# Performance work log

Hardware: AMD Instinct MI355X
Metric: run time of the kernel (lower is better)

Reference implementation:

```python
import jax, jax.numpy as jnp
import numpy as np

N, E = 10000, 320000
MUL0, MUL1 = 64, 32  # 64x0e + 32x1o
SQ3 = 3.0 ** 0.5
SQ2 = 2.0 ** 0.5


def ssp(v):  # shifted softplus
    return jax.nn.softplus(v) - jnp.log(2.0)


def mlp2(v, W1, W2):  # e3nn FullyConnectedNet style: /sqrt(fan_in), no bias, act between
    h = ssp(v @ (W1 / jnp.sqrt(1.0 * W1.shape[0])))
    return h @ (W2 / jnp.sqrt(1.0 * W2.shape[0]))


def linear_rs(x0, x1, W0, b0, W1):  # per-irrep-type linear with 1/sqrt(fan_in) rescale
    y0 = x0 @ (W0 / jnp.sqrt(1.0 * W0.shape[0])) + b0
    y1 = jnp.einsum('nui,uv->nvi', x1, W1) / jnp.sqrt(1.0 * W1.shape[0])
    return y0, y1


def forward(x, edge_sh, edge_attr, W0p, b0p, W1p, W0n, b0n, W1n, G1, g1b, G2, g2b, F1, F2, L1, L2, WO0, bO0, WO1, WO2, edge_index):
    dst, src = edge_index[0], edge_index[1]
    x0 = x[:, :MUL0]                      # [N,64] scalars
    x1 = x[:, MUL0:].reshape(N, MUL1, 3)  # [N,32,3] l=1 vectors
    # linear_node_pre, then invariant edge features s0 (scalars of dst/src + l1 inner products)
    p0, p1 = linear_rs(x0, x1, W0p, b0p, W1p)
    ip1 = jnp.sum(p1[dst] * p1[src], -1) / SQ3          # [E,32]
    s0 = jnp.concatenate([p0[dst], p0[src], ip1], -1)   # [E,160]
    # NormGate: gate scalars + l1 norms through a 2-layer SiLU MLP
    n1 = jnp.sqrt(jnp.sum(x1 * x1, -1) + 1e-12)         # [N,32]
    f0 = jnp.concatenate([x0, n1], -1)                  # [N,96]
    g = jax.nn.silu(f0 @ G1 + g1b) @ G2 + g2b           # [N,96]
    x0g, x1g = g[:, :MUL0], x1 * g[:, MUL0:, None]
    # linear_node
    x0n, x1n = linear_rs(x0g, x1g, W0n, b0n, W1n)
    # per-edge tensor-product weights: fc_node(edge_attr) * layer_l0(s0)
    w = mlp2(edge_attr, F1, F2) * mlp2(s0, L1, L2)      # [E,224]
    w1, w2, w3, w4, w5 = w[:, :64], w[:, 64:128], w[:, 128:160], w[:, 160:192], w[:, 192:224]
    xs0, xs1 = x0n[src], x1n[src]                       # gather source nodes
    sh0, sh1 = edge_sh[:, 0], edge_sh[:, 1:4]
    # depthwise 'uvu' tensor product paths (w3j constants for l<=1)
    o0a = w1 * xs0 * sh0[:, None]                                        # (0e,0e)->0e  [E,64]
    o0b = w4 * jnp.sum(xs1 * sh1[:, None, :], -1) / SQ3                  # (1o,1o)->0e  [E,32]
    o1a = w2[:, :, None] * xs0[:, :, None] * sh1[:, None, :] / SQ3       # (0e,1o)->1o  [E,64,3]
    o1b = w3[:, :, None] * xs1 * sh0[:, None, None]                      # (1o,0e)->1o  [E,32,3]
    o1c = w5[:, :, None] * jnp.cross(xs1, jnp.broadcast_to(sh1[:, None, :], xs1.shape)) / SQ2  # (1o,1o)->1e [E,32,3]
    ef = jnp.concatenate([o0a, o0b, o1a.reshape(E, -1), o1b.reshape(E, -1), o1c.reshape(E, -1)], -1)  # [E,480]
    out = jax.ops.segment_sum(ef, dst, num_segments=N)  # scatter-add over dst
    # linear_out: 96x0e + 96x1o + 32x1e -> 128x0e + 64x1o + 32x1e
    t0 = out[:, :96]
    t1 = out[:, 96:384].reshape(N, 96, 3)
    t2 = out[:, 384:].reshape(N, 32, 3)
    y0 = t0 @ (WO0 / jnp.sqrt(96.0)) + bO0
    y1 = jnp.einsum('nui,uv->nvi', t1, WO1) / jnp.sqrt(96.0)
    y2 = jnp.einsum('nui,uv->nvi', t2, WO2) / jnp.sqrt(32.0)
    return jnp.concatenate([y0, y1.reshape(N, -1), y2.reshape(N, -1)], -1)  # [N,416]


def setup_inputs():
    key = jax.random.key(0)
    ks = jax.random.split(key, 20)
    rn = lambda k, s: jax.random.normal(k, s, dtype=jnp.float32)
    z = lambda n: jnp.zeros((n,), jnp.float32)
    return dict(
        x=rn(ks[0], (N, 160)),
        edge_sh=rn(ks[1], (E, 4)),
        edge_attr=rn(ks[2], (E, 32)),
        W0p=rn(ks[3], (64, 64)), b0p=z(64), W1p=rn(ks[4], (32, 32)),
        W0n=rn(ks[5], (64, 64)), b0n=z(64), W1n=rn(ks[6], (32, 32)),
        G1=rn(ks[7], (96, 96)) / 96 ** 0.5, g1b=z(96),
        G2=rn(ks[8], (96, 96)) / 96 ** 0.5, g2b=z(96),
        F1=rn(ks[9], (32, 32)), F2=rn(ks[10], (32, 224)),
        L1=rn(ks[11], (160, 32)), L2=rn(ks[12], (32, 224)),
        WO0=rn(ks[13], (96, 128)), bO0=z(128),
        WO1=rn(ks[14], (96, 64)), WO2=rn(ks[15], (32, 32)),
        edge_index=jax.random.randint(ks[16], (2, E), 0, N),
    )


def reference(x, edge_sh, edge_attr, W0p, b0p, W1p, W0n, b0n, W1n, G1, g1b, G2, g2b, F1, F2, L1, L2, WO0, bO0, WO1, WO2, edge_index):
    return forward(x, edge_sh, edge_attr, W0p, b0p, W1p, W0n, b0n, W1n, G1, g1b, G2, g2b, F1, F2, L1, L2, WO0, bO0, WO1, WO2, edge_index)
```

## Files before the change

kernel.cpp:

```cpp
#include <hip/hip_runtime.h>
#include <math.h>

#define NN 10000
#define EE 320000
#define TILE 32

constexpr float INVS32  = 0.17677669529663687f;
constexpr float INVS160 = 0.07905694150420949f;
constexpr float INVS96  = 0.10206207261596575f;
constexpr float INVS3   = 0.5773502691896258f;
constexpr float INVS2   = 0.7071067811865476f;
constexpr float LN2     = 0.6931471805599453f;

typedef short bf16x8 __attribute__((ext_vector_type(8)));
typedef float f32x4  __attribute__((ext_vector_type(4)));

__device__ __forceinline__ float sspf(float v) {
  return fmaxf(v, 0.f) + __logf(1.f + __expf(-fabsf(v))) - LN2;
}
__device__ __forceinline__ ushort f2bf(float f) {
  union { float f; unsigned u; } v; v.f = f;
  unsigned r = v.u + 0x7FFF + ((v.u >> 16) & 1);
  return (ushort)(r >> 16);
}
__device__ __forceinline__ float bf2f(ushort u) {
  return __uint_as_float(((unsigned)u) << 16);
}
__device__ __forceinline__ unsigned pk(float a, float b) {
  return (unsigned)f2bf(a) | ((unsigned)f2bf(b) << 16);
}

__global__ __launch_bounds__(1024) void scan_k(const int* __restrict__ cnt,
                                               int* __restrict__ cursor) {
  __shared__ int s[1024];
  const int t = threadIdx.x;
  int loc[10];
  int sum = 0;
#pragma unroll
  for (int jj = 0; jj < 10; ++jj) {
    int idx = t * 10 + jj;
    int c = (idx < NN) ? cnt[idx] : 0;
    loc[jj] = sum;
    sum += c;
  }
  s[t] = sum;
  __syncthreads();
  for (int d = 1; d < 1024; d <<= 1) {
    int v = (t >= d) ? s[t - d] : 0;
    __syncthreads();
    s[t] += v;
    __syncthreads();
  }
  const int excl = (t > 0) ? s[t - 1] : 0;
#pragma unroll
  for (int jj = 0; jj < 10; ++jj) {
    int idx = t * 10 + jj;
    if (idx < NN) cursor[idx] = excl + loc[jj];
  }
}

__global__ void prep_t_k(const float* __restrict__ F2, const float* __restrict__ L2,
                         const float* __restrict__ WO0, const float* __restrict__ WO1,
                         const float* __restrict__ WO2,
                         const float* __restrict__ F1, const float* __restrict__ L1,
                         const int* __restrict__ ei, int* __restrict__ cnt,
                         ushort* __restrict__ F2Tb, ushort* __restrict__ L2Tb,
                         float* __restrict__ WO0T, float* __restrict__ WO1T,
                         float* __restrict__ WO2T,
                         ushort* __restrict__ F1Tb, ushort* __restrict__ L1cTb) {
  int i = blockIdx.x * 256 + threadIdx.x;
  if (i < EE) atomicAdd(&cnt[ei[i]], 1);
  if (i < 7168) {
    int c = i >> 5, k = i & 31;
    float sc = (c < 64)  ? (1.f / 32.f)
             : (c < 128) ? (INVS3 / 32.f)
             : (c < 160) ? (1.f / 32.f)
             : (c < 192) ? (INVS3 / 32.f)
                         : (INVS2 / 32.f);
    F2Tb[i] = f2bf(F2[k * 224 + c] * sc);
    L2Tb[i] = f2bf(L2[k * 224 + c]);
  } else if (i < 7168 + 12288) {
    int j = i - 7168; int k = j / 96, u = j - k * 96;
    WO0T[j] = WO0[u * 128 + k] * INVS96;
  } else if (i < 7168 + 12288 + 6144) {
    int j = i - 7168 - 12288; int v = j / 96, u = j - v * 96;
    WO1T[j] = WO1[u * 64 + v] * INVS96;
  } else if (i < 7168 + 12288 + 6144 + 1024) {
    int j = i - 7168 - 12288 - 6144; int v = j >> 5, u = j & 31;
    WO2T[j] = WO2[u * 32 + v] * INVS32;
  } else if (i < 26624 + 1024) {
    int j = i - 26624; int n = j >> 5, k = j & 31;
    F1Tb[j] = f2bf(F1[k * 32 + n] * INVS32);
  } else if (i < 27648 + 1024) {
    int j = i - 27648; int n = j >> 5, k = j & 31;
    L1cTb[j] = f2bf(L1[(128 + k) * 32 + n] * INVS160);
  }
}

__global__ __launch_bounds__(64) void node_prep_k(
    const float* __restrict__ x,
    const float* __restrict__ W0p, const float* __restrict__ b0p,
    const float* __restrict__ W1p,
    const float* __restrict__ W0n, const float* __restrict__ b0n,
    const float* __restrict__ W1n,
    const float* __restrict__ G1, const float* __restrict__ g1b,
    const float* __restrict__ G2, const float* __restrict__ g2b,
    const float* __restrict__ L1,
    const int* __restrict__ ei, int* __restrict__ cursor, int* __restrict__ order,
    float* __restrict__ p1w, ushort* __restrict__ x0nb, ushort* __restrict__ x1nb,
    float* __restrict__ Aw, float* __restrict__ Bw)
{
  {
    int gid = blockIdx.x * 64 + threadIdx.x;
#pragma unroll
    for (int r = 0; r < 2; ++r) {
      int e = gid + r * 160000;
      int p = atomicAdd(&cursor[ei[e]], 1);
      order[p] = e;
    }
  }

  const int lane = threadIdx.x;
  const int nb = blockIdx.x * 4;

  __shared__ float sX[4][160];
  __shared__ float sP0[4][64];
  __shared__ float sF0[4][96];
  __shared__ float sH1[4][96];
  __shared__ float sG[4][96];

#pragma unroll
  for (int j = 0; j < 4; ++j) {
    const int n = nb + j;
    sX[j][lane]      = x[n * 160 + lane];
    sX[j][lane + 64] = x[n * 160 + lane + 64];
    if (lane < 32) sX[j][lane + 128] = x[n * 160 + lane + 128];
  }

  {
    float a0 = 0.f, a1 = 0.f, a2 = 0.f, a3 = 0.f;
    for (int i = 0; i < 64; ++i) {
      const float w = W0p[i * 64 + lane];
      a0 = fmaf(sX[0][i], w, a0); a1 = fmaf(sX[1][i], w, a1);
      a2 = fmaf(sX[2][i], w, a2); a3 = fmaf(sX[3][i], w, a3);
    }
    const float b = b0p[lane];
    sP0[0][lane] = a0 * 0.125f + b; sP0[1][lane] = a1 * 0.125f + b;
    sP0[2][lane] = a2 * 0.125f + b; sP0[3][lane] = a3 * 0.125f + b;
#pragma unroll
    for (int j = 0; j < 4; ++j) sF0[j][lane] = sX[j][lane];
  }

  {
    const int o = lane; const int v = o / 3, i_ = o - 3 * v;
    float a0 = 0.f, a1 = 0.f, a2 = 0.f, a3 = 0.f;
    for (int u = 0; u < 32; ++u) {
      const float w = W1p[u * 32 + v];
      a0 = fmaf(sX[0][64 + u * 3 + i_], w, a0);
      a1 = fmaf(sX[1][64 + u * 3 + i_], w, a1);
      a2 = fmaf(sX[2][64 + u * 3 + i_], w, a2);
      a3 = fmaf(sX[3][64 + u * 3 + i_], w, a3);
    }
    p1w[(size_t)(nb + 0) * 96 + o] = a0 * INVS32;
    p1w[(size_t)(nb + 1) * 96 + o] = a1 * INVS32;
    p1w[(size_t)(nb + 2) * 96 + o] = a2 * INVS32;
    p1w[(size_t)(nb + 3) * 96 + o] = a3 * INVS32;
  }
  if (lane < 32) {
    const int o = 64 + lane; const int v = o / 3, i_ = o - 3 * v;
    float a0 = 0.f, a1 = 0.f, a2 = 0.f, a3 = 0.f;
    for (int u = 0; u < 32; ++u) {
      const float w = W1p[u * 32 + v];
      a0 = fmaf(sX[0][64 + u * 3 + i_], w, a0);
      a1 = fmaf(sX[1][64 + u * 3 + i_], w, a1);
      a2 = fmaf(sX[2][64 + u * 3 + i_], w, a2);
      a3 = fmaf(sX[3][64 + u * 3 + i_], w, a3);
    }
    p1w[(size_t)(nb + 0) * 96 + o] = a0 * INVS32;
    p1w[(size_t)(nb + 1) * 96 + o] = a1 * INVS32;
    p1w[(size_t)(nb + 2) * 96 + o] = a2 * INVS32;
    p1w[(size_t)(nb + 3) * 96 + o] = a3 * INVS32;
  }

  if (lane < 32) {
#pragma unroll
    for (int j = 0; j < 4; ++j) {
      float s2 = 1e-12f;
#pragma unroll
      for (int i = 0; i < 3; ++i) { float t = sX[j][64 + lane * 3 + i]; s2 += t * t; }
      sF0[j][64 + lane] = sqrtf(s2);
    }
  }

  {
    const float b = g1b[lane];
    float a0 = b, a1 = b, a2 = b, a3 = b;
    for (int i = 0; i < 96; ++i) {
      const float w = G1[i * 96 + lane];
      a0 = fmaf(sF0[0][i], w, a0); a1 = fmaf(sF0[1][i], w, a1);
      a2 = fmaf(sF0[2][i], w, a2); a3 = fmaf(sF0[3][i], w, a3);
    }
    sH1[0][lane] = a0 / (1.f + __expf(-a0));
    sH1[1][lane] = a1 / (1.f + __expf(-a1));
    sH1[2][lane] = a2 / (1.f + __expf(-a2));
    sH1[3][lane] = a3 / (1.f + __expf(-a3));
  }
  if (lane < 32) {
    const int o = 64 + lane;
    const float b = g1b[o];
    float a0 = b, a1 = b, a2 = b, a3 = b;
    for (int i = 0; i < 96; ++i) {
      const float w = G1[i * 96 + o];
      a0 = fmaf(sF0[0][i], w, a0); a1 = fmaf(sF0[1][i], w, a1);
      a2 = fmaf(sF0[2][i], w, a2); a3 = fmaf(sF0[3][i], w, a3);
    }
    sH1[0][o] = a0 / (1.f + __expf(-a0));
    sH1[1][o] = a1 / (1.f + __expf(-a1));
    sH1[2][o] = a2 / (1.f + __expf(-a2));
    sH1[3][o] = a3 / (1.f + __expf(-a3));
  }

  {
    const float b = g2b[lane];
    float a0 = b, a1 = b, a2 = b, a3 = b;
    for (int i = 0; i < 96; ++i) {
      const float w = G2[i * 96 + lane];
      a0 = fmaf(sH1[0][i], w, a0); a1 = fmaf(sH1[1][i], w, a1);
      a2 = fmaf(sH1[2][i], w, a2); a3 = fmaf(sH1[3][i], w, a3);
    }
    sG[0][lane] = a0; sG[1][lane] = a1; sG[2][lane] = a2; sG[3][lane] = a3;
  }
  if (lane < 32) {
    const int o = 64 + lane;
    const float b = g2b[o];
    float a0 = b, a1 = b, a2 = b, a3 = b;
    for (int i = 0; i < 96; ++i) {
      const float w = G2[i * 96 + o];
      a0 = fmaf(sH1[0][i], w, a0); a1 = fmaf(sH1[1][i], w, a1);
      a2 = fmaf(sH1[2][i], w, a2); a3 = fmaf(sH1[3][i], w, a3);
    }
    sG[0][o] = a0; sG[1][o] = a1; sG[2][o] = a2; sG[3][o] = a3;
  }

  {
    float a0 = 0.f, a1 = 0.f, a2 = 0.f, a3 = 0.f;
    for (int i = 0; i < 64; ++i) {
      const float w = W0n[i * 64 + lane];
      a0 = fmaf(sG[0][i], w, a0); a1 = fmaf(sG[1][i], w, a1);
      a2 = fmaf(sG[2][i], w, a2); a3 = fmaf(sG[3][i], w, a3);
    }
    const float b = b0n[lane];
    x0nb[(size_t)(nb + 0) * 64 + lane] = f2bf(a0 * 0.125f + b);
    x0nb[(size_t)(nb + 1) * 64 + lane] = f2bf(a1 * 0.125f + b);
    x0nb[(size_t)(nb + 2) * 64 + lane] = f2bf(a2 * 0.125f + b);
    x0nb[(size_t)(nb + 3) * 64 + lane] = f2bf(a3 * 0.125f + b);
  }

  {
    const int o = lane; const int v = o / 3, i_ = o - 3 * v;
    float a0 = 0.f, a1 = 0.f, a2 = 0.f, a3 = 0.f;
    for (int u = 0; u < 32; ++u) {
      const float w = W1n[u * 32 + v];
      a0 = fmaf(sX[0][64 + u * 3 + i_] * sG[0][64 + u], w, a0);
      a1 = fmaf(sX[1][64 + u * 3 + i_] * sG[1][64 + u], w, a1);
      a2 = fmaf(sX[2][64 + u * 3 + i_] * sG[2][64 + u], w, a2);
      a3 = fmaf(sX[3][64 + u * 3 + i_] * sG[3][64 + u], w, a3);
    }
    x1nb[(size_t)(nb + 0) * 96 + o] = f2bf(a0 * INVS32);
    x1nb[(size_t)(nb + 1) * 96 + o] = f2bf(a1 * INVS32);
    x1nb[(size_t)(nb + 2) * 96 + o] = f2bf(a2 * INVS32);
    x1nb[(size_t)(nb + 3) * 96 + o] = f2bf(a3 * INVS32);
  }
  if (lane < 32) {
    const int o = 64 + lane; const int v = o / 3, i_ = o - 3 * v;
    float a0 = 0.f, a1 = 0.f, a2 = 0.f, a3 = 0.f;
    for (int u = 0; u < 32; ++u) {
      const float w = W1n[u * 32 + v];
      a0 = fmaf(sX[0][64 + u * 3 + i_] * sG[0][64 + u], w, a0);
      a1 = fmaf(sX[1][64 + u * 3 + i_] * sG[1][64 + u], w, a1);
      a2 = fmaf(sX[2][64 + u * 3 + i_] * sG[2][64 + u], w, a2);
      a3 = fmaf(sX[3][64 + u * 3 + i_] * sG[3][64 + u], w, a3);
    }
    x1nb[(size_t)(nb + 0) * 96 + o] = f2bf(a0 * INVS32);
    x1nb[(size_t)(nb + 1) * 96 + o] = f2bf(a1 * INVS32);
    x1nb[(size_t)(nb + 2) * 96 + o] = f2bf(a2 * INVS32);
    x1nb[(size_t)(nb + 3) * 96 + o] = f2bf(a3 * INVS32);
  }

  if (lane < 32) {
    float a0 = 0.f, a1 = 0.f, a2 = 0.f, a3 = 0.f;
    float c0 = 0.f, c1 = 0.f, c2 = 0.f, c3 = 0.f;
    for (int i = 0; i < 64; ++i) {
      const float wa = L1[i * 32 + lane];
      const float wb = L1[(64 + i) * 32 + lane];
      a0 = fmaf(sP0[0][i], wa, a0); a1 = fmaf(sP0[1][i], wa, a1);
      a2 = fmaf(sP0[2][i], wa, a2); a3 = fmaf(sP0[3][i], wa, a3);
      c0 = fmaf(sP0[0][i], wb, c0); c1 = fmaf(sP0[1][i], wb, c1);
      c2 = fmaf(sP0[2][i], wb, c2); c3 = fmaf(sP0[3][i], wb, c3);
    }
    Aw[(size_t)(nb + 0) * 32 + lane] = a0 * INVS160;
    Aw[(size_t)(nb + 1) * 32 + lane] = a1 * INVS160;
    Aw[(size_t)(nb + 2) * 32 + lane] = a2 * INVS160;
    Aw[(size_t)(nb + 3) * 32 + lane] = a3 * INVS160;
    Bw[(size_t)(nb + 0) * 32 + lane] = c0 * INVS160;
    Bw[(size_t)(nb + 1) * 32 + lane] = c1 * INVS160;
    Bw[(size_t)(nb + 2) * 32 + lane] = c2 * INVS160;
    Bw[(size_t)(nb + 3) * 32 + lane] = c3 * INVS160;
  }
}

__global__ __launch_bounds__(256, 4) void fused_edge_k(
    const float* __restrict__ edge_attr,
    const float* __restrict__ edge_sh,
    const int* __restrict__ ei,
    const ushort* __restrict__ F1Tb, const ushort* __restrict__ L1cTb,
    const ushort* __restrict__ F2Tb, const ushort* __restrict__ L2Tb,
    const float* __restrict__ p1w, const float* __restrict__ Aw,
    const float* __restrict__ Bw,
    const ushort* __restrict__ x0nb, const ushort* __restrict__ x1nb,
    const int* __restrict__ order,
    float* __restrict__ o480)
{
  const int s0  = blockIdx.x * TILE;
  const int tid = threadIdx.x;

  __shared__ __align__(16) char uMem[32 * 224 * 2];
  ushort (*sW)[224] = (ushort (*)[224])uMem;
  ushort* sEAb = (ushort*)uMem;
  ushort* sIPb = (ushort*)(uMem + 2560);
  float*  sAB  = (float*)(uMem + 5120);

  __shared__ ushort sHF[32][40];
  __shared__ ushort sHL[32][40];
  __shared__ ushort sXS0[32][64];
  __shared__ ushort sXS1[32][96];
  __shared__ __align__(16) float sSH[32][4];
  __shared__ int    sDst[32];

  const int g = tid >> 3, l = tid & 7;
  const int e   = order[s0 + g];
  const int dst = ei[e];
  const int src = ei[EE + e];
  if (l == 0) sDst[g] = dst;

  {
    float4 ea = *(const float4*)(edge_attr + (size_t)e * 32 + l * 4);
    *(unsigned*)&sEAb[g * 40 + l * 4 + 0] = pk(ea.x, ea.y);
    *(unsigned*)&sEAb[g * 40 + l * 4 + 2] = pk(ea.z, ea.w);
  }
  if (l == 1) *(float4*)&sSH[g][0] = *(const float4*)(edge_sh + (size_t)e * 4);
  {
    uint4 v = *(const uint4*)(x0nb + (size_t)src * 64 + l * 8);
    *(uint4*)&sXS0[g][l * 8] = v;
    const uint2* b2 = (const uint2*)(x1nb + (size_t)src * 96 + l * 12);
    uint2 w0 = b2[0], w1 = b2[1], w2 = b2[2];
    *(uint2*)&sXS1[g][l * 12 + 0] = w0;
    *(uint2*)&sXS1[g][l * 12 + 4] = w1;
    *(uint2*)&sXS1[g][l * 12 + 8] = w2;
  }
  {
    const float4* pd = (const float4*)(p1w + (size_t)dst * 96 + l * 12);
    const float4* ps = (const float4*)(p1w + (size_t)src * 96 + l * 12);
    float dp[12], sp[12];
#pragma unroll
    for (int k = 0; k < 3; ++k) {
      float4 v = pd[k]; dp[4*k] = v.x; dp[4*k+1] = v.y; dp[4*k+2] = v.z; dp[4*k+3] = v.w;
      float4 u = ps[k]; sp[4*k] = u.x; sp[4*k+1] = u.y; sp[4*k+2] = u.z; sp[4*k+3] = u.w;
    }
    float ip[4];
#pragma unroll
    for (int vv = 0; vv < 4; ++vv) {
      const int b = 3 * vv;
      ip[vv] = (dp[b] * sp[b] + dp[b+1] * sp[b+1] + dp[b+2] * sp[b+2]) * INVS3;
    }
    *(unsigned*)&sIPb[g * 40 + l * 4 + 0] = pk(ip[0], ip[1]);
    *(unsigned*)&sIPb[g * 40 + l * 4 + 2] = pk(ip[2], ip[3]);
  }
  {
    float4 av = *(const float4*)(Aw + (size_t)dst * 32 + l * 4);
    float4 bv = *(const float4*)(Bw + (size_t)src * 32 + l * 4);
    f32x4 ab;
    ab[0] = av.x + bv.x; ab[1] = av.y + bv.y;
    ab[2] = av.z + bv.z; ab[3] = av.w + bv.w;
    *(f32x4*)&sAB[g * 36 + l * 4] = ab;
  }
  __syncthreads();

  {
    const int wvi  = tid >> 6;
    const int lane = tid & 63;
    const int r = lane & 15;
    const int h = lane >> 4;
    const int qt = wvi & 1;
    const bool isHL = (wvi >= 2);
    const ushort* aBase = isHL ? sIPb : sEAb;
    const ushort* bW    = isHL ? L1cTb : F1Tb;
    ushort* outB = isHL ? &sHL[0][0] : &sHF[0][0];
    bf16x8 afr = *(const bf16x8*)&aBase[(qt * 16 + r) * 40 + h * 8];
#pragma unroll
    for (int ct = 0; ct < 2; ++ct) {
      const int c = ct * 16 + r;
      bf16x8 bfr = *(const bf16x8*)&bW[c * 32 + h * 8];
      f32x4 z = {0.f, 0.f, 0.f, 0.f};
      f32x4 o = __builtin_amdgcn_mfma_f32_16x16x32_bf16(afr, bfr, z, 0, 0, 0);
#pragma unroll
      for (int i = 0; i < 4; ++i) {
        const int q = qt * 16 + h * 4 + i;
        float v = o[i];
        if (isHL) v += sAB[q * 36 + c];
        outB[q * 40 + c] = f2bf(sspf(v));
      }
    }
  }
  __syncthreads();

  {
    const int wv   = tid >> 6;
    const int lane = tid & 63;
    const int r = lane & 15;
    const int h = lane >> 4;
    bf16x8 aF0 = *(const bf16x8*)&sHF[r][h * 8];
    bf16x8 aF1 = *(const bf16x8*)&sHF[16 + r][h * 8];
    bf16x8 aL0 = *(const bf16x8*)&sHL[r][h * 8];
    bf16x8 aL1 = *(const bf16x8*)&sHL[16 + r][h * 8];
    const int ct0 = (wv < 2) ? wv * 4 : 8 + (wv - 2) * 3;
    const int nct = (wv < 2) ? 4 : 3;
    for (int t = 0; t < nct; ++t) {
      const int ct = ct0 + t;
      const int c  = ct * 16 + r;
      bf16x8 bF = *(const bf16x8*)&F2Tb[c * 32 + h * 8];
      bf16x8 bL = *(const bf16x8*)&L2Tb[c * 32 + h * 8];
      f32x4 z = {0.f, 0.f, 0.f, 0.f};
      f32x4 wf0 = __builtin_amdgcn_mfma_f32_16x16x32_bf16(aF0, bF, z, 0, 0, 0);
      f32x4 wl0 = __builtin_amdgcn_mfma_f32_16x16x32_bf16(aL0, bL, z, 0, 0, 0);
      f32x4 wf1 = __builtin_amdgcn_mfma_f32_16x16x32_bf16(aF1, bF, z, 0, 0, 0);
      f32x4 wl1 = __builtin_amdgcn_mfma_f32_16x16x32_bf16(aL1, bL, z, 0, 0, 0);
#pragma unroll
      for (int i = 0; i < 4; ++i) {
        sW[h * 4 + i][c]      = f2bf(wf0[i] * wl0[i]);
        sW[16 + h * 4 + i][c] = f2bf(wf1[i] * wl1[i]);
      }
    }
  }
  __syncthreads();

  {
    const int h  = tid >> 7;
    const int tl = tid & 127;
    const int q0 = h * 16;
    float a0 = 0.f, a1 = 0.f, a2 = 0.f, a3 = 0.f;

    for (int q = q0; q < q0 + 16; ++q) {
      const float4 sh = *(const float4*)&sSH[q][0];
      if (tl < 64) {
        const float x0 = bf2f(sXS0[q][tl]);
        const float w0 = bf2f(sW[q][tl]);
        const float w1 = bf2f(sW[q][64 + tl]);
        a0 = fmaf(w0 * x0, sh.x, a0);
        const float t = w1 * x0;
        a1 = fmaf(t, sh.y, a1);
        a2 = fmaf(t, sh.z, a2);
        a3 = fmaf(t, sh.w, a3);
      } else if (tl < 96) {
        const int c = tl - 64;
        const float x0v = bf2f(sXS1[q][3 * c + 0]);
        const float x1v = bf2f(sXS1[q][3 * c + 1]);
        const float x2v = bf2f(sXS1[q][3 * c + 2]);
        const float wb = bf2f(sW[q][160 + c]);
        const float wd = bf2f(sW[q][128 + c]);
        const float d = fmaf(x2v, sh.w, fmaf(x1v, sh.z, x0v * sh.y));
        a0 = fmaf(wb, d, a0);
        const float t = wd * sh.x;
        a1 = fmaf(t, x0v, a1);
        a2 = fmaf(t, x1v, a2);
        a3 = fmaf(t, x2v, a3);
      } else {
        const int u = tl - 96;
        const float x0v = bf2f(sXS1[q][3 * u + 0]);
        const float x1v = bf2f(sXS1[q][3 * u + 1]);
        const float x2v = bf2f(sXS1[q][3 * u + 2]);
        const float wc = bf2f(sW[q][192 + u]);
        a0 = fmaf(wc, fmaf(x1v, sh.w, -(x2v * sh.z)), a0);
        a1 = fmaf(wc, fmaf(x2v, sh.y, -(x0v * sh.w)), a1);
        a2 = fmaf(wc, fmaf(x0v, sh.z, -(x1v * sh.y)), a2);
      }
      const int d = sDst[q];
      const bool fl = (q == q0 + 15) || (sDst[q + 1] != d);
      if (fl) {
        float* dp = o480 + (size_t)d * 480;
        if (tl < 64) {
          atomicAdd(dp + tl, a0);
          atomicAdd(dp + 96 + 3 * tl + 0, a1);
          atomicAdd(dp + 96 + 3 * tl + 1, a2);
          atomicAdd(dp + 96 + 3 * tl + 2, a3);
        } else if (tl < 96) {
          const int c = tl - 64;
          atomicAdd(dp + 64 + c, a0);
          atomicAdd(dp + 288 + 3 * c + 0, a1);
          atomicAdd(dp + 288 + 3 * c + 1, a2);
          atomicAdd(dp + 288 + 3 * c + 2, a3);
        } else {
          const int u = tl - 96;
          atomicAdd(dp + 384 + 3 * u + 0, a0);
          atomicAdd(dp + 384 + 3 * u + 1, a1);
          atomicAdd(dp + 384 + 3 * u + 2, a2);
        }
        a0 = 0.f; a1 = 0.f; a2 = 0.f; a3 = 0.f;
      }
    }
  }
}

__global__ __launch_bounds__(64) void out_wo_k(
    const float* __restrict__ o480,
    const float* __restrict__ WO0T, const float* __restrict__ WO1T,
    const float* __restrict__ WO2T, const float* __restrict__ bO0,
    float* __restrict__ out)
{
  const int lane = threadIdx.x;
  const int nb = blockIdx.x * 4;
  __shared__ float sO[4][480];
#pragma unroll
  for (int j = 0; j < 4; ++j) {
    const float4* src = (const float4*)(o480 + (size_t)(nb + j) * 480);
    for (int idx = lane; idx < 120; idx += 64)
      *(float4*)&sO[j][idx * 4] = src[idx];
  }

  for (int k = lane; k < 416; k += 64) {
    float y0, y1, y2, y3;
    if (k < 128) {
      const float* wr = WO0T + k * 96;
      float a0 = 0.f, a1 = 0.f, a2 = 0.f, a3 = 0.f;
      for (int u = 0; u < 96; ++u) {
        const float w = wr[u];
        a0 = fmaf(w, sO[0][u], a0); a1 = fmaf(w, sO[1][u], a1);
        a2 = fmaf(w, sO[2][u], a2); a3 = fmaf(w, sO[3][u], a3);
      }
      const float b = bO0[k];
      y0 = a0 + b; y1 = a1 + b; y2 = a2 + b; y3 = a3 + b;
    } else if (k < 320) {
      const int kk = k - 128; const int v = kk / 3; const int i = kk - 3 * v;
      const float* wr = WO1T + v * 96;
      float a0 = 0.f, a1 = 0.f, a2 = 0.f, a3 = 0.f;
      for (int u = 0; u < 96; ++u) {
        const float w = wr[u];
        a0 = fmaf(w, sO[0][96 + u * 3 + i], a0);
        a1 = fmaf(w, sO[1][96 + u * 3 + i], a1);
        a2 = fmaf(w, sO[2][96 + u * 3 + i], a2);
        a3 = fmaf(w, sO[3][96 + u * 3 + i], a3);
      }
      y0 = a0; y1 = a1; y2 = a2; y3 = a3;
    } else {
      const int kk = k - 320; const int v = kk / 3; const int i = kk - 3 * v;
      const float* wr = WO2T + v * 32;
      float a0 = 0.f, a1 = 0.f, a2 = 0.f, a3 = 0.f;
      for (int u = 0; u < 32; ++u) {
        const float w = wr[u];
        a0 = fmaf(w, sO[0][384 + u * 3 + i], a0);
        a1 = fmaf(w, sO[1][384 + u * 3 + i], a1);
        a2 = fmaf(w, sO[2][384 + u * 3 + i], a2);
        a3 = fmaf(w, sO[3][384 + u * 3 + i], a3);
      }
      y0 = a0; y1 = a1; y2 = a2; y3 = a3;
    }
    out[(size_t)(nb + 0) * 416 + k] = y0;
    out[(size_t)(nb + 1) * 416 + k] = y1;
    out[(size_t)(nb + 2) * 416 + k] = y2;
    out[(size_t)(nb + 3) * 416 + k] = y3;
  }
}

extern "C" void kernel_launch(void* const* d_in, const int* in_sizes, int n_in,
                              void* d_out, int out_size, void* d_ws, size_t ws_size,
                              hipStream_t stream) {
  const float* x         = (const float*)d_in[0];
  const float* edge_sh   = (const float*)d_in[1];
  const float* edge_attr = (const float*)d_in[2];
  const float* W0p       = (const float*)d_in[3];
  const float* b0p       = (const float*)d_in[4];
  const float* W1p       = (const float*)d_in[5];
  const float* W0n       = (const float*)d_in[6];
  const float* b0n       = (const float*)d_in[7];
  const float* W1n       = (const float*)d_in[8];
  const float* G1        = (const float*)d_in[9];
  const float* g1b       = (const float*)d_in[10];
  const float* G2        = (const float*)d_in[11];
  const float* g2b       = (const float*)d_in[12];
  const float* F1        = (const float*)d_in[13];
  const float* F2        = (const float*)d_in[14];
  const float* L1        = (const float*)d_in[15];
  const float* L2        = (const float*)d_in[16];
  const float* WO0       = (const float*)d_in[17];
  const float* bO0       = (const float*)d_in[18];
  const float* WO1       = (const float*)d_in[19];
  const float* WO2       = (const float*)d_in[20];
  const int*   ei        = (const int*)d_in[21];
  float* out = (float*)d_out;

  float*  p1w  = (float*)d_ws;
  ushort* x0nb = (ushort*)(p1w + NN * 96);
  ushort* x1nb = x0nb + NN * 64;
  float*  Aw   = (float*)(x1nb + NN * 96);
  float*  Bw   = Aw + NN * 32;
  float*  o480 = Bw + NN * 32;
  int* cnt    = (int*)(o480 + (size_t)NN * 480);
  int* cursor = cnt    + NN;
  int* order  = cursor + NN;
  uintptr_t p = (uintptr_t)(order + EE);
  p = (p + 15) & ~(uintptr_t)15;
  ushort* F2Tb  = (ushort*)p;
  ushort* L2Tb  = F2Tb + 224 * 32;
  ushort* F1Tb  = L2Tb + 224 * 32;
  ushort* L1cTb = F1Tb + 32 * 32;
  uintptr_t p2 = (uintptr_t)(L1cTb + 32 * 32);
  p2 = (p2 + 15) & ~(uintptr_t)15;
  float* WO0T = (float*)p2;
  float* WO1T = WO0T + 128 * 96;
  float* WO2T = WO1T + 64 * 96;

  hipMemsetAsync(cnt, 0, NN * sizeof(int), stream);
  hipMemsetAsync(o480, 0, (size_t)NN * 480 * sizeof(float), stream);
  prep_t_k<<<(EE + 255) / 256, 256, 0, stream>>>(F2, L2, WO0, WO1, WO2, F1, L1,
                                                 ei, cnt,
                                                 F2Tb, L2Tb, WO0T, WO1T, WO2T,
                                                 F1Tb, L1cTb);
  scan_k<<<1, 1024, 0, stream>>>(cnt, cursor);
  node_prep_k<<<NN / 4, 64, 0, stream>>>(x, W0p, b0p, W1p, W0n, b0n, W1n,
                                         G1, g1b, G2, g2b, L1,
                                         ei, cursor, order,
                                         p1w, x0nb, x1nb, Aw, Bw);
  fused_edge_k<<<EE / TILE, 256, 0, stream>>>(edge_attr, edge_sh, ei,
                                              F1Tb, L1cTb, F2Tb, L2Tb,
                                              p1w, Aw, Bw, x0nb, x1nb,
                                              order, o480);
  out_wo_k<<<NN / 4, 64, 0, stream>>>(o480, WO0T, WO1T, WO2T, bO0, out);
}
```

Before: 324.1 us.

## Use component-planar aggregation layout and single-half edge scatter loop

Reorders the per-node 480-float aggregation buffer into component-planar blocks so every lane's atomic adds go to contiguous addresses (dp+tl, dp+128+tl, ...), and updates the output linear kernel's indexing to match. The scatter phase now runs on only the first 128 threads over all 32 edges of the tile instead of two halves of 16 edges each. This gives coalesced atomics and fewer flushes when consecutive edges share a destination, but leaves half the block idle during accumulation.

Result: faster. 285.4 us (-11.9%).

```diff
diff --git a/kernel.cpp b/kernel.cpp
--- a/kernel.cpp
+++ b/kernel.cpp
@@ -319,7 +319,7 @@
     const float* __restrict__ Bw,
     const ushort* __restrict__ x0nb, const ushort* __restrict__ x1nb,
     const int* __restrict__ order,
-    float* __restrict__ o480)
+    float* __restrict__ o480p)
 {
   const int s0  = blockIdx.x * TILE;
   const int tid = threadIdx.x;
@@ -444,13 +444,11 @@
   }
   __syncthreads();
 
-  {
-    const int h  = tid >> 7;
-    const int tl = tid & 127;
-    const int q0 = h * 16;
-    float a0 = 0.f, a1 = 0.f, a2 = 0.f, a3 = 0.f;
-
-    for (int q = q0; q < q0 + 16; ++q) {
+  if (tid < 128) {
+    const int tl = tid;
+    float a0 = 0.f, a1 = 0.f, a2 = 0.f, a3 = 0.f;
+
+    for (int q = 0; q < TILE; ++q) {
       const float4 sh = *(const float4*)&sSH[q][0];
       if (tl < 64) {
         const float x0 = bf2f(sXS0[q][tl]);
@@ -485,26 +483,13 @@
         a2 = fmaf(wc, fmaf(x0v, sh.z, -(x1v * sh.y)), a2);
       }
       const int d = sDst[q];
-      const bool fl = (q == q0 + 15) || (sDst[q + 1] != d);
+      const bool fl = (q == TILE - 1) || (sDst[q + 1] != d);
       if (fl) {
-        float* dp = o480 + (size_t)d * 480;
-        if (tl < 64) {
-          atomicAdd(dp + tl, a0);
-          atomicAdd(dp + 96 + 3 * tl + 0, a1);
-          atomicAdd(dp + 96 + 3 * tl + 1, a2);
-          atomicAdd(dp + 96 + 3 * tl + 2, a3);
-        } else if (tl < 96) {
-          const int c = tl - 64;
-          atomicAdd(dp + 64 + c, a0);
-          atomicAdd(dp + 288 + 3 * c + 0, a1);
-          atomicAdd(dp + 288 + 3 * c + 1, a2);
-          atomicAdd(dp + 288 + 3 * c + 2, a3);
-        } else {
-          const int u = tl - 96;
-          atomicAdd(dp + 384 + 3 * u + 0, a0);
-          atomicAdd(dp + 384 + 3 * u + 1, a1);
-          atomicAdd(dp + 384 + 3 * u + 2, a2);
-        }
+        float* dp = o480p + (size_t)d * 480;
+        atomicAdd(dp + tl, a0);
+        atomicAdd(dp + 128 + tl, a1);
+        atomicAdd(dp + 256 + tl, a2);
+        if (tl < 96) atomicAdd(dp + 384 + tl, a3);
         a0 = 0.f; a1 = 0.f; a2 = 0.f; a3 = 0.f;
       }
     }
@@ -512,7 +497,7 @@
 }
 
 __global__ __launch_bounds__(64) void out_wo_k(
-    const float* __restrict__ o480,
+    const float* __restrict__ o480p,
     const float* __restrict__ WO0T, const float* __restrict__ WO1T,
     const float* __restrict__ WO2T, const float* __restrict__ bO0,
     float* __restrict__ out)
@@ -522,7 +507,7 @@
   __shared__ float sO[4][480];
 #pragma unroll
   for (int j = 0; j < 4; ++j) {
-    const float4* src = (const float4*)(o480 + (size_t)(nb + j) * 480);
+    const float4* src = (const float4*)(o480p + (size_t)(nb + j) * 480);
     for (int idx = lane; idx < 120; idx += 64)
       *(float4*)&sO[j][idx * 4] = src[idx];
   }
@@ -542,25 +527,27 @@
     } else if (k < 320) {
       const int kk = k - 128; const int v = kk / 3; const int i = kk - 3 * v;
       const float* wr = WO1T + v * 96;
+      const int base = 128 + 128 * i;
       float a0 = 0.f, a1 = 0.f, a2 = 0.f, a3 = 0.f;
       for (int u = 0; u < 96; ++u) {
         const float w = wr[u];
-        a0 = fmaf(w, sO[0][96 + u * 3 + i], a0);
-        a1 = fmaf(w, sO[1][96 + u * 3 + i], a1);
-        a2 = fmaf(w, sO[2][96 + u * 3 + i], a2);
-        a3 = fmaf(w, sO[3][96 + u * 3 + i], a3);
+        a0 = fmaf(w, sO[0][base + u], a0);
+        a1 = fmaf(w, sO[1][base + u], a1);
+        a2 = fmaf(w, sO[2][base + u], a2);
+        a3 = fmaf(w, sO[3][base + u], a3);
       }
       y0 = a0; y1 = a1; y2 = a2; y3 = a3;
     } else {
       const int kk = k - 320; const int v = kk / 3; const int i = kk - 3 * v;
       const float* wr = WO2T + v * 32;
+      const int base = 96 + 128 * i;
       float a0 = 0.f, a1 = 0.f, a2 = 0.f, a3 = 0.f;
       for (int u = 0; u < 32; ++u) {
         const float w = wr[u];
-        a0 = fmaf(w, sO[0][384 + u * 3 + i], a0);
-        a1 = fmaf(w, sO[1][384 + u * 3 + i], a1);
-        a2 = fmaf(w, sO[2][384 + u * 3 + i], a2);
-        a3 = fmaf(w, sO[3][384 + u * 3 + i], a3);
+        a0 = fmaf(w, sO[0][base + u], a0);
+        a1 = fmaf(w, sO[1][base + u], a1);
+        a2 = fmaf(w, sO[2][base + u], a2);
+        a3 = fmaf(w, sO[3][base + u], a3);
       }
       y0 = a0; y1 = a1; y2 = a2; y3 = a3;
     }
```
